# Optimization experiments

Measured on AMD Instinct MI355X. Metric: run time of the kernel, lower is better.

Reference implementation:

```python
import jax, jax.numpy as jnp
import numpy as np

TOP_K = 2
NUM_EXPERTS = 8
CAPACITY_FACTOR = 1.0


def setup_inputs() -> dict:
    key = jax.random.key(0)
    k1, k2, k3, k4 = jax.random.split(key, 4)
    sl, bs, hs, ffn = 2048, 2, 1024, 4096
    x = jax.random.normal(k1, (sl, bs, hs), dtype=jnp.float32)
    router_w = jax.random.normal(k2, (hs, NUM_EXPERTS), dtype=jnp.float32) * 0.02
    w1 = jax.random.normal(k3, (NUM_EXPERTS, hs, ffn), dtype=jnp.float32) * 0.02
    w2 = jax.random.normal(k4, (NUM_EXPERTS, ffn, hs), dtype=jnp.float32) * 0.02
    bias = jnp.zeros((1, 1, hs), dtype=jnp.float32)
    return {"x": x, "router_w": router_w, "w1": w1, "w2": w2, "bias": bias}


def _moe_forward(x, router_w, w1, w2):
    sl, bs, hs = x.shape
    xf = x.reshape(-1, hs)                                   # [T, H]
    T = xf.shape[0]
    TK = T * TOP_K
    capacity = int(CAPACITY_FACTOR * TOP_K * T / NUM_EXPERTS)  # static

    # Router: softmax over experts, then top-k (LearnedRouter)
    scores = jax.nn.softmax(xf @ router_w, axis=-1)          # [T, E]
    expert_weights, top_experts = jax.lax.top_k(scores, TOP_K)  # [T, K]
    ew = expert_weights.reshape(-1)                          # [T*K]
    te = top_experts.reshape(-1).astype(jnp.int32)           # [T*K]

    # indices_and_bins: stable sort by expert id + histogram + inclusive cumsum
    indices = jnp.argsort(te, stable=True)                   # sorted pos -> flat slot
    tokens_per_expert = jnp.zeros((NUM_EXPERTS,), jnp.int32).at[te].add(1)
    bins = jnp.cumsum(tokens_per_expert)                     # inclusive cumsum
    starts = bins - tokens_per_expert                        # exclusive offsets

    # binned_gather -> [E, capacity, H]; tokens beyond capacity are dropped
    c_range = jnp.arange(capacity)
    pos = starts[:, None] + c_range[None, :]                 # [E, C] positions in sorted order
    valid = c_range[None, :] < tokens_per_expert[:, None]    # [E, C]
    slot = indices[jnp.clip(pos, 0, TK - 1)]                 # flat (token*K + k) slot
    tok = slot // TOP_K                                      # source token row
    gathered = jnp.where(valid[..., None], xf[tok], 0.0)     # [E, C, H]

    # grouped expert MLP: gelu(x @ w1) @ w2  (megablocks mlp.MLP)
    h = jax.nn.gelu(jnp.einsum('ech,ehf->ecf', gathered, w1))
    y = jnp.einsum('ecf,efh->ech', h, w2)                    # [E, C, H]

    # binned_scatter: weighted accumulate back to token rows
    p = jnp.arange(TK)
    e_of_p = jnp.searchsorted(bins, p, side='right')         # expert of sorted pos
    c_of_p = p - starts[e_of_p]                              # slot within expert bin
    ok = c_of_p < capacity                                   # dropped tokens contribute 0
    vals = jnp.where(ok[:, None], y[e_of_p, jnp.clip(c_of_p, 0, capacity - 1)], 0.0)
    flat = indices                                           # flat slot at sorted pos p
    w = ew[flat]
    out = jnp.zeros((T, hs), x.dtype).at[flat // TOP_K].add(w[:, None] * vals)
    return out.reshape(sl, bs, hs)


def reference(x, router_w, w1, w2, bias):
    out = _moe_forward(x, router_w, w1, w2)
    return (out, bias)
```

## Files before the change

kernel.cpp:

```cpp
#include <hip/hip_runtime.h>
#include <hip/hip_bf16.h>


#define T_TOK 4096
#define HS 1024
#define FFN 4096
#define NE 8
#define CAP 1024
#define TKS 8192

#define WS_TE   67108864
#define WS_EW   67141632
#define WS_PERM 67174400
#define WS_WT   67239936
#define WS_XB   134348800

typedef float f4 __attribute__((ext_vector_type(4)));
typedef __bf16 bf16x8 __attribute__((ext_vector_type(8)));
typedef float f32x4 __attribute__((ext_vector_type(4)));

__device__ __forceinline__ void gld_lds16(const void* g, void* l) {
    __builtin_amdgcn_global_load_lds(
        (const __attribute__((address_space(1))) unsigned int*)g,
        (__attribute__((address_space(3))) unsigned int*)l, 16, 0, 0);
}

__global__ void init_out_kernel(float* __restrict__ out, const float* __restrict__ bias) {
    int i = blockIdx.x * 256 + threadIdx.x;
    const int TH = T_TOK * HS;
    if (i < TH) out[i] = 0.0f;
    else if (i < TH + HS) out[i] = bias[i - TH];
}

__global__ __launch_bounds__(256) void router_kernel(const float* __restrict__ x,
                                                     const float* __restrict__ rw,
                                                     int* __restrict__ te,
                                                     float* __restrict__ ew,
                                                     __bf16* __restrict__ xb) {
    __shared__ float rwt[NE * HS];
    int tid = threadIdx.x;
    for (int i = tid; i < NE * HS; i += 256) {
        int h = i >> 3, e = i & 7;
        rwt[e * HS + h] = rw[i];
    }
    __syncthreads();
    int wave = tid >> 6, lane = tid & 63;
    int t = blockIdx.x * 4 + wave;
    const float* xr = x + (size_t)t * HS;
    float s[NE];
    float xv[16];
#pragma unroll
    for (int e = 0; e < NE; ++e) s[e] = 0.0f;
#pragma unroll
    for (int j = 0; j < 16; ++j) {
        int h = lane + j * 64;
        xv[j] = xr[h];
#pragma unroll
        for (int e = 0; e < NE; ++e) s[e] += xv[j] * rwt[e * HS + h];
    }
#pragma unroll
    for (int j = 0; j < 16; ++j)
        xb[(size_t)t * HS + lane + j * 64] = (__bf16)xv[j];
#pragma unroll
    for (int e = 0; e < NE; ++e) {
#pragma unroll
        for (int off = 1; off < 64; off <<= 1) s[e] += __shfl_xor(s[e], off, 64);
    }
    float m = s[0];
#pragma unroll
    for (int e = 1; e < NE; ++e) m = fmaxf(m, s[e]);
    float psum = 0.0f;
#pragma unroll
    for (int e = 0; e < NE; ++e) psum += __expf(s[e] - m);
    int e0 = 0; float v0 = s[0];
#pragma unroll
    for (int e = 1; e < NE; ++e) { if (s[e] > v0) { v0 = s[e]; e0 = e; } }
    int e1 = -1; float v1 = -1e30f;
#pragma unroll
    for (int e = 0; e < NE; ++e) { if (e != e0 && s[e] > v1) { v1 = s[e]; e1 = e; } }
    if (lane == 0) {
        float inv = 1.0f / psum;
        te[2 * t]     = e0;
        te[2 * t + 1] = e1;
        ew[2 * t]     = __expf(v0 - m) * inv;
        ew[2 * t + 1] = __expf(v1 - m) * inv;
    }
}

__global__ __launch_bounds__(256) void sort_kernel(const int* __restrict__ te,
                                                   int* __restrict__ perm) {
    __shared__ int hist[256 * NE];
    int tid = threadIdx.x;
#pragma unroll
    for (int e = 0; e < NE; ++e) hist[tid * NE + e] = 0;
    for (int i = tid; i < TKS; i += 256) perm[i] = -1;
    __syncthreads();
    for (int j = 0; j < 32; ++j) {
        int p = tid * 32 + j;
        hist[tid * NE + te[p]]++;
    }
    __syncthreads();
    if (tid < NE) {
        int run = 0;
        for (int i = 0; i < 256; ++i) {
            int v = hist[i * NE + tid];
            hist[i * NE + tid] = run;
            run += v;
        }
    }
    __syncthreads();
    for (int j = 0; j < 32; ++j) {
        int p = tid * 32 + j;
        int e = te[p];
        int c = hist[tid * NE + e]++;
        if (c < CAP) perm[e * CAP + c] = p;
    }
}

__global__ __launch_bounds__(256) void conv_wt_kernel(const float* __restrict__ w,
                                                      __bf16* __restrict__ wt,
                                                      int K, int N) {
    __shared__ __bf16 t[64][72];
    const int e = blockIdx.z;
    const int kb = blockIdx.y * 64, nb = blockIdx.x * 64;
    const int tid = threadIdx.x;
    const float* src = w + ((size_t)e * K + kb) * N + nb;
    {
        const int kk = tid >> 4, nc = (tid & 15) * 4;
#pragma unroll
        for (int i = 0; i < 4; ++i) {
            int k = kk + 16 * i;
            f4 v = *(const f4*)(src + (size_t)k * N + nc);
            t[nc + 0][k] = (__bf16)v[0];
            t[nc + 1][k] = (__bf16)v[1];
            t[nc + 2][k] = (__bf16)v[2];
            t[nc + 3][k] = (__bf16)v[3];
        }
    }
    __syncthreads();
    __bf16* dst = wt + ((size_t)e * N + nb) * K + kb;
    const int nn = tid >> 3, ch = (tid & 7) * 8;
#pragma unroll
    for (int i = 0; i < 2; ++i) {
        int n = nn + 32 * i;
        bf16x8 v = *(const bf16x8*)(&t[n][ch]);
        *(bf16x8*)(dst + (size_t)n * K + ch) = v;
    }
}


#define STAGE8(c_, koff_) do {                                              \
    _Pragma("unroll")                                                       \
    for (int j = 0; j < 4; ++j) {                                           \
        gld_lds16(aptr[j] + (koff_), &As[c_][j * 64 + w * 8][0]);           \
        gld_lds16(bptr[j] + (koff_), &Bs[c_][j * 64 + w * 8][0]);           \
    }                                                                       \
} while (0)

#define TILE_BODY(c_) do {                                                  \
    _Pragma("unroll")                                                       \
    for (int kk = 0; kk < 2; ++kk) {                                        \
        const int g = (kk * 4 + (lane >> 4)) ^ (lane & 7);                  \
        bf16x8 af[8], bb[4];                                                \
        _Pragma("unroll")                                                   \
        for (int mi = 0; mi < 8; ++mi)                                      \
            af[mi] = *(const bf16x8*)&As[c_][wr * 128 + mi * 16 + l15][g * 8]; \
        _Pragma("unroll")                                                   \
        for (int ni = 0; ni < 4; ++ni)                                      \
            bb[ni] = *(const bf16x8*)&Bs[c_][wc * 64 + ni * 16 + l15][g * 8]; \
        __builtin_amdgcn_s_setprio(1);                                      \
        _Pragma("unroll")                                                   \
        for (int mi = 0; mi < 8; ++mi)                                      \
            _Pragma("unroll")                                               \
            for (int ni = 0; ni < 4; ++ni)                                  \
                acc[mi][ni] = __builtin_amdgcn_mfma_f32_16x16x32_bf16(      \
                    af[mi], bb[ni], acc[mi][ni], 0, 0, 0);                  \
        __builtin_amdgcn_s_setprio(0);                                      \
    }                                                                       \
} while (0)

#define KTILE_SYNC() do {                                                   \
    asm volatile("s_waitcnt vmcnt(0)" ::: "memory");                        \
    __builtin_amdgcn_s_barrier();                                           \
    asm volatile("" ::: "memory");                                          \
} while (0)

__global__ __launch_bounds__(512, 2) void gemm1_kernel(const __bf16* __restrict__ xb,
                                                       const __bf16* __restrict__ w1t,
                                                       const int* __restrict__ perm,
                                                       __bf16* __restrict__ hbuf) {
    __shared__ __bf16 As[2][256][64];
    __shared__ __bf16 Bs[2][256][64];
    const int e = blockIdx.z, mblk = blockIdx.y, nblk = blockIdx.x;
    const int tid = threadIdx.x, lane = tid & 63, w = tid >> 6;
    const int wr = w >> 2, wc = w & 3;
    const int l15 = lane & 15;
    const int srl = lane >> 3;
    const int gsrc = (lane & 7) ^ srl;

    const __bf16* aptr[4];
    const __bf16* bptr[4];
#pragma unroll
    for (int j = 0; j < 4; ++j) {
        int arow = j * 64 + w * 8 + srl;
        int p = perm[e * CAP + mblk * 256 + arow];
        int tok = (p < 0) ? 0 : (p >> 1);
        aptr[j] = xb + (size_t)tok * HS + gsrc * 8;
        int brow = nblk * 256 + j * 64 + w * 8 + srl;
        bptr[j] = w1t + ((size_t)e * FFN + brow) * HS + gsrc * 8;
    }

    f32x4 acc[8][4];
#pragma unroll
    for (int mi = 0; mi < 8; ++mi)
#pragma unroll
        for (int ni = 0; ni < 4; ++ni) acc[mi][ni] = (f32x4)0.0f;

    const int NT = HS / 64;
    STAGE8(0, 0);
    KTILE_SYNC();
    int c = 0;
    for (int t = 0; t < NT; ++t) {
        if (t + 1 < NT) STAGE8(c ^ 1, (t + 1) * 64);
        TILE_BODY(c);
        KTILE_SYNC();
        c ^= 1;
    }

    const int mbase = mblk * 256 + wr * 128;
    const int nbase = nblk * 256 + wc * 64;
#pragma unroll
    for (int mi = 0; mi < 8; ++mi) {
#pragma unroll
        for (int ni = 0; ni < 4; ++ni) {
#pragma unroll
            for (int reg = 0; reg < 4; ++reg) {
                int mrow = mbase + mi * 16 + (lane >> 4) * 4 + reg;
                int ncol = nbase + ni * 16 + l15;
                float z = acc[mi][ni][reg];
                float u = 0.7978845608028654f * (z + 0.044715f * z * z * z);
                float tt = 1.0f - 2.0f / (1.0f + __expf(2.0f * u));
                float gv = 0.5f * z * (1.0f + tt);
                hbuf[(size_t)(e * CAP + mrow) * FFN + ncol] = (__bf16)gv;
            }
        }
    }
}

__global__ __launch_bounds__(512, 2) void gemm2_kernel(const __bf16* __restrict__ hbuf,
                                                       const __bf16* __restrict__ w2t,
                                                       const int* __restrict__ perm,
                                                       const float* __restrict__ ew,
                                                       float* __restrict__ out) {
    __shared__ __bf16 As[2][256][64];
    __shared__ __bf16 Bs[2][256][64];
    const int e = blockIdx.z & 7, half = blockIdx.z >> 3;
    const int mblk = blockIdx.y, nblk = blockIdx.x;
    const int tid = threadIdx.x, lane = tid & 63, w = tid >> 6;
    const int wr = w >> 2, wc = w & 3;
    const int l15 = lane & 15;
    const int srl = lane >> 3;
    const int gsrc = (lane & 7) ^ srl;

    const __bf16* aptr[4];
    const __bf16* bptr[4];
#pragma unroll
    for (int j = 0; j < 4; ++j) {
        int arow = j * 64 + w * 8 + srl;
        aptr[j] = hbuf + ((size_t)(e * CAP + mblk * 256 + arow)) * FFN
                  + (size_t)half * 2048 + gsrc * 8;
        int brow = nblk * 256 + j * 64 + w * 8 + srl;
        bptr[j] = w2t + ((size_t)e * HS + brow) * FFN
                  + (size_t)half * 2048 + gsrc * 8;
    }

    f32x4 acc[8][4];
#pragma unroll
    for (int mi = 0; mi < 8; ++mi)
#pragma unroll
        for (int ni = 0; ni < 4; ++ni) acc[mi][ni] = (f32x4)0.0f;

    const int NT = 2048 / 64;
    STAGE8(0, 0);
    KTILE_SYNC();
    int c = 0;
    for (int t = 0; t < NT; ++t) {
        if (t + 1 < NT) STAGE8(c ^ 1, (t + 1) * 64);
        TILE_BODY(c);
        KTILE_SYNC();
        c ^= 1;
    }

    int* sperm = (int*)&As[0][0][0];
    float* swt = (float*)(sperm + 256);
    if (tid < 256) {
        int p = perm[e * CAP + mblk * 256 + tid];
        sperm[tid] = p;
        swt[tid] = (p >= 0) ? ew[p] : 0.0f;
    }
    __syncthreads();

    const int nbase = nblk * 256 + wc * 64;
#pragma unroll
    for (int mi = 0; mi < 8; ++mi) {
#pragma unroll
        for (int reg = 0; reg < 4; ++reg) {
            int mloc = wr * 128 + mi * 16 + (lane >> 4) * 4 + reg;
            int p = sperm[mloc];
            if (p >= 0) {
                int tok = p >> 1;
                float wgt = swt[mloc];
#pragma unroll
                for (int ni = 0; ni < 4; ++ni) {
                    int n = nbase + ni * 16 + l15;
                    atomicAdd(&out[(size_t)tok * HS + n], wgt * acc[mi][ni][reg]);
                }
            }
        }
    }
}

extern "C" void kernel_launch(void* const* d_in, const int* in_sizes, int n_in,
                              void* d_out, int out_size, void* d_ws, size_t ws_size,
                              hipStream_t stream) {
    const float* x    = (const float*)d_in[0];
    const float* rw   = (const float*)d_in[1];
    const float* w1   = (const float*)d_in[2];
    const float* w2   = (const float*)d_in[3];
    const float* bias = (const float*)d_in[4];
    float* out = (float*)d_out;
    char* ws = (char*)d_ws;

    __bf16* hbuf = (__bf16*)ws;
    int*    te   = (int*)(ws + WS_TE);
    float*  ew   = (float*)(ws + WS_EW);
    int*    perm = (int*)(ws + WS_PERM);
    __bf16* wt   = (__bf16*)(ws + WS_WT);
    __bf16* xb   = (__bf16*)(ws + WS_XB);

    hipLaunchKernelGGL(init_out_kernel, dim3((T_TOK * HS + HS + 255) / 256), dim3(256),
                       0, stream, out, bias);
    hipLaunchKernelGGL(router_kernel, dim3(T_TOK / 4), dim3(256), 0, stream,
                       x, rw, te, ew, xb);
    hipLaunchKernelGGL(sort_kernel, dim3(1), dim3(256), 0, stream, te, perm);
    hipLaunchKernelGGL(conv_wt_kernel, dim3(FFN / 64, HS / 64, NE), dim3(256),
                       0, stream, w1, wt, HS, FFN);
    hipLaunchKernelGGL(gemm1_kernel, dim3(FFN / 256, CAP / 256, NE), dim3(512),
                       0, stream, xb, wt, perm, hbuf);
    hipLaunchKernelGGL(conv_wt_kernel, dim3(HS / 64, FFN / 64, NE), dim3(256),
                       0, stream, w2, wt, FFN, HS);
    hipLaunchKernelGGL(gemm2_kernel, dim3(HS / 256, CAP / 256, NE * 2), dim3(512),
                       0, stream, hbuf, wt, perm, ew, out);
}
```

Baseline: 309.8 us.

## Interleave staged LDS loads with MFMA quadrants in a finer-grained K-loop pipeline

Replaces the simple double-buffered K loop with a schedule that splits each tile into four MFMA quadrants. A and B half-tile global-to-LDS loads are issued between the quadrants, A is prefetched two tiles ahead, and barriers plus partial vmcnt waits order the steps. The aim is to hide memory latency behind matrix math instead of waiting for all loads at each tile boundary. It also rewrites the GELU tanh form as an equivalent sigmoid form using a fast reciprocal. The extra barriers and tighter register use could add sync overhead or hurt scheduling.

```diff
diff --git a/kernel.cpp b/kernel.cpp
--- a/kernel.cpp
+++ b/kernel.cpp
@@ -149,41 +149,88 @@
 }
 
 
-#define STAGE8(c_, koff_) do {                                              \
-    _Pragma("unroll")                                                       \
-    for (int j = 0; j < 4; ++j) {                                           \
-        gld_lds16(aptr[j] + (koff_), &As[c_][j * 64 + w * 8][0]);           \
-        gld_lds16(bptr[j] + (koff_), &Bs[c_][j * 64 + w * 8][0]);           \
-    }                                                                       \
-} while (0)
-
-#define TILE_BODY(c_) do {                                                  \
-    _Pragma("unroll")                                                       \
-    for (int kk = 0; kk < 2; ++kk) {                                        \
-        const int g = (kk * 4 + (lane >> 4)) ^ (lane & 7);                  \
-        bf16x8 af[8], bb[4];                                                \
-        _Pragma("unroll")                                                   \
-        for (int mi = 0; mi < 8; ++mi)                                      \
-            af[mi] = *(const bf16x8*)&As[c_][wr * 128 + mi * 16 + l15][g * 8]; \
-        _Pragma("unroll")                                                   \
-        for (int ni = 0; ni < 4; ++ni)                                      \
-            bb[ni] = *(const bf16x8*)&Bs[c_][wc * 64 + ni * 16 + l15][g * 8]; \
-        __builtin_amdgcn_s_setprio(1);                                      \
-        _Pragma("unroll")                                                   \
-        for (int mi = 0; mi < 8; ++mi)                                      \
-            _Pragma("unroll")                                               \
-            for (int ni = 0; ni < 4; ++ni)                                  \
-                acc[mi][ni] = __builtin_amdgcn_mfma_f32_16x16x32_bf16(      \
-                    af[mi], bb[ni], acc[mi][ni], 0, 0, 0);                  \
-        __builtin_amdgcn_s_setprio(0);                                      \
-    }                                                                       \
-} while (0)
-
-#define KTILE_SYNC() do {                                                   \
-    asm volatile("s_waitcnt vmcnt(0)" ::: "memory");                        \
+#define PBAR() do {                                                         \
+    asm volatile("" ::: "memory");                                          \
     __builtin_amdgcn_s_barrier();                                           \
     asm volatile("" ::: "memory");                                          \
 } while (0)
+
+#define WAITV(N_) asm volatile("s_waitcnt vmcnt(" #N_ ")" ::: "memory")
+
+#define STAGE_A(cb_, h_, koff_) do {                                        \
+    gld_lds16(aptr[(h_)*2 + 0] + (koff_), &As[cb_][(h_)*128 + w*16 + 0][0]);\
+    gld_lds16(aptr[(h_)*2 + 1] + (koff_), &As[cb_][(h_)*128 + w*16 + 8][0]);\
+} while (0)
+
+#define STAGE_B(cb_, h_, koff_) do {                                        \
+    gld_lds16(bptr[(h_)*2 + 0] + (koff_), &Bs[cb_][(h_)*128 + w*16 + 0][0]);\
+    gld_lds16(bptr[(h_)*2 + 1] + (koff_), &Bs[cb_][(h_)*128 + w*16 + 8][0]);\
+} while (0)
+
+#define RD_A4(MB_) do {                                                     \
+    _Pragma("unroll")                                                       \
+    for (int mi = 0; mi < 4; ++mi)                                          \
+        _Pragma("unroll")                                                   \
+        for (int kk = 0; kk < 2; ++kk)                                      \
+            a[mi][kk] = *(const bf16x8*)&As[c][wr*128 + ((MB_)+mi)*16 + l15]\
+                            [((kk*4 + (lane>>4)) ^ (lane&7)) * 8];          \
+} while (0)
+
+#define RD_B2(NB_) do {                                                     \
+    _Pragma("unroll")                                                       \
+    for (int ni = 0; ni < 2; ++ni)                                          \
+        _Pragma("unroll")                                                   \
+        for (int kk = 0; kk < 2; ++kk)                                      \
+            b[(NB_)+ni][kk] = *(const bf16x8*)&Bs[c][wc*64 + ((NB_)+ni)*16 + l15]\
+                            [((kk*4 + (lane>>4)) ^ (lane&7)) * 8];          \
+} while (0)
+
+#define MFMA16(MB_, NB_) do {                                               \
+    __builtin_amdgcn_s_setprio(1);                                          \
+    _Pragma("unroll")                                                       \
+    for (int mi = 0; mi < 4; ++mi)                                          \
+        _Pragma("unroll")                                                   \
+        for (int ni = 0; ni < 2; ++ni)                                      \
+            _Pragma("unroll")                                               \
+            for (int kk = 0; kk < 2; ++kk)                                  \
+                acc[(MB_)+mi][(NB_)+ni] = __builtin_amdgcn_mfma_f32_16x16x32_bf16(\
+                    a[mi][kk], b[(NB_)+ni][kk], acc[(MB_)+mi][(NB_)+ni], 0, 0, 0);\
+    __builtin_amdgcn_s_setprio(0);                                          \
+} while (0)
+
+#define KLOOP(NT_)                                                          \
+    STAGE_A(0, 0, 0); STAGE_A(0, 1, 0);                                     \
+    STAGE_B(0, 0, 0); STAGE_B(0, 1, 0);                                     \
+    STAGE_A(1, 0, 64); STAGE_A(1, 1, 64);                                   \
+    for (int t = 0; t < (NT_); ++t) {                                       \
+        const int c = t & 1;                                                \
+        if (t == (NT_) - 1) WAITV(0); else WAITV(4);                        \
+        PBAR();                                                             \
+                                                               \
+        RD_A4(0); RD_B2(0);                                                 \
+        if (t + 1 < (NT_)) STAGE_B(c ^ 1, 0, (t + 1) * 64);                 \
+        PBAR();                                                             \
+        MFMA16(0, 0);                                                       \
+        PBAR();                                                             \
+                                                               \
+        RD_B2(2);                                                           \
+        if (t + 1 < (NT_)) STAGE_B(c ^ 1, 1, (t + 1) * 64);                 \
+        PBAR();                                                             \
+        MFMA16(0, 2);                                                       \
+        PBAR();                                                             \
+                                                               \
+        RD_A4(4);                                                           \
+        PBAR();                                                             \
+        MFMA16(4, 2);                                                       \
+        PBAR();                                                             \
+                                                               \
+        if (t + 2 < (NT_)) { STAGE_A(c, 0, (t + 2) * 64);                   \
+                             STAGE_A(c, 1, (t + 2) * 64); }                 \
+        PBAR();                                                             \
+        __builtin_amdgcn_sched_barrier(0);                                  \
+        MFMA16(4, 0);                                                       \
+        PBAR();                                                             \
+    }
 
 __global__ __launch_bounds__(512, 2) void gemm1_kernel(const __bf16* __restrict__ xb,
                                                        const __bf16* __restrict__ w1t,
@@ -201,13 +248,16 @@
     const __bf16* aptr[4];
     const __bf16* bptr[4];
 #pragma unroll
-    for (int j = 0; j < 4; ++j) {
-        int arow = j * 64 + w * 8 + srl;
-        int p = perm[e * CAP + mblk * 256 + arow];
-        int tok = (p < 0) ? 0 : (p >> 1);
-        aptr[j] = xb + (size_t)tok * HS + gsrc * 8;
-        int brow = nblk * 256 + j * 64 + w * 8 + srl;
-        bptr[j] = w1t + ((size_t)e * FFN + brow) * HS + gsrc * 8;
+    for (int h = 0; h < 2; ++h) {
+#pragma unroll
+        for (int o = 0; o < 2; ++o) {
+            int r = h * 128 + w * 16 + o * 8 + srl;
+            int p = perm[e * CAP + mblk * 256 + r];
+            int tok = (p < 0) ? 0 : (p >> 1);
+            aptr[h * 2 + o] = xb + (size_t)tok * HS + gsrc * 8;
+            int brow = nblk * 256 + r;
+            bptr[h * 2 + o] = w1t + ((size_t)e * FFN + brow) * HS + gsrc * 8;
+        }
     }
 
     f32x4 acc[8][4];
@@ -215,17 +265,9 @@
     for (int mi = 0; mi < 8; ++mi)
 #pragma unroll
         for (int ni = 0; ni < 4; ++ni) acc[mi][ni] = (f32x4)0.0f;
-
-    const int NT = HS / 64;
-    STAGE8(0, 0);
-    KTILE_SYNC();
-    int c = 0;
-    for (int t = 0; t < NT; ++t) {
-        if (t + 1 < NT) STAGE8(c ^ 1, (t + 1) * 64);
-        TILE_BODY(c);
-        KTILE_SYNC();
-        c ^= 1;
-    }
+    bf16x8 a[4][2], b[4][2];
+
+    KLOOP(HS / 64)
 
     const int mbase = mblk * 256 + wr * 128;
     const int nbase = nblk * 256 + wc * 64;
@@ -238,9 +280,10 @@
                 int mrow = mbase + mi * 16 + (lane >> 4) * 4 + reg;
                 int ncol = nbase + ni * 16 + l15;
                 float z = acc[mi][ni][reg];
-                float u = 0.7978845608028654f * (z + 0.044715f * z * z * z);
-                float tt = 1.0f - 2.0f / (1.0f + __expf(2.0f * u));
-                float gv = 0.5f * z * (1.0f + tt);
+                float z2 = z * z;
+                float y = z * (1.5957691216057308f + 0.07135481627f * z2);
+                float ex = __expf(-y);
+                float gv = z * __builtin_amdgcn_rcpf(1.0f + ex);
                 hbuf[(size_t)(e * CAP + mrow) * FFN + ncol] = (__bf16)gv;
             }
         }
@@ -261,17 +304,21 @@
     const int l15 = lane & 15;
     const int srl = lane >> 3;
     const int gsrc = (lane & 7) ^ srl;
+    const size_t kbase = (size_t)half * 2048;
 
     const __bf16* aptr[4];
     const __bf16* bptr[4];
 #pragma unroll
-    for (int j = 0; j < 4; ++j) {
-        int arow = j * 64 + w * 8 + srl;
-        aptr[j] = hbuf + ((size_t)(e * CAP + mblk * 256 + arow)) * FFN
-                  + (size_t)half * 2048 + gsrc * 8;
-        int brow = nblk * 256 + j * 64 + w * 8 + srl;
-        bptr[j] = w2t + ((size_t)e * HS + brow) * FFN
-                  + (size_t)half * 2048 + gsrc * 8;
+    for (int h = 0; h < 2; ++h) {
+#pragma unroll
+        for (int o = 0; o < 2; ++o) {
+            int r = h * 128 + w * 16 + o * 8 + srl;
+            aptr[h * 2 + o] = hbuf + ((size_t)(e * CAP + mblk * 256 + r)) * FFN
+                              + kbase + gsrc * 8;
+            int brow = nblk * 256 + r;
+            bptr[h * 2 + o] = w2t + ((size_t)e * HS + brow) * FFN
+                              + kbase + gsrc * 8;
+        }
     }
 
     f32x4 acc[8][4];
@@ -279,18 +326,11 @@
     for (int mi = 0; mi < 8; ++mi)
 #pragma unroll
         for (int ni = 0; ni < 4; ++ni) acc[mi][ni] = (f32x4)0.0f;
-
-    const int NT = 2048 / 64;
-    STAGE8(0, 0);
-    KTILE_SYNC();
-    int c = 0;
-    for (int t = 0; t < NT; ++t) {
-        if (t + 1 < NT) STAGE8(c ^ 1, (t + 1) * 64);
-        TILE_BODY(c);
-        KTILE_SYNC();
-        c ^= 1;
-    }
-
+    bf16x8 a[4][2], b[4][2];
+
+    KLOOP(2048 / 64)
+
+    __syncthreads();
     int* sperm = (int*)&As[0][0][0];
     float* swt = (float*)(sperm + 256);
     if (tid < 256) {
```

Result: faster. 289.1 us (-6.7%).
